# Kernel tuning notes

Hardware: AMD Instinct MI355X
Metric: run time of the kernel (lower is better)

Reference implementation:

```python
import jax, jax.numpy as jnp
import numpy as np

B, L, D = 32, 8192, 256
M = L // 2 + 1  # max possible valley count (strict local minima can't be adjacent)


def setup_inputs() -> dict:
    key = jax.random.key(0)
    k1, k2, k3 = jax.random.split(key, 3)
    xs_pad = jax.random.normal(k1, (B, L, D), dtype=jnp.float32)
    olens = jax.random.randint(k2, (B,), 1, L + 1, dtype=jnp.int32)
    # linear_sigmoid params: Linear(256, 1)
    W = jax.random.normal(k3, (D, 1), dtype=jnp.float32) * 0.05
    b = jnp.zeros((1,), dtype=jnp.float32)
    return {"xs_pad": xs_pad, "olens": olens, "W": W, "b": b}


def reference(xs_pad, olens, W, b):
    Bq, Lq, Dq = xs_pad.shape
    # scalar importance: sigmoid(Linear(x))  [B, L, 1]
    s = jax.nn.sigmoid(xs_pad @ W + b)
    alpha_h = s * xs_pad                       # [B, L, D]
    sq = s[..., 0]                             # [B, L]
    # shifted neighbors, zero-padded at the ends (matches F.pad of the detached scalars)
    s_before = jnp.pad(sq[:, :-1], ((0, 0), (1, 0)))
    s_after = jnp.pad(sq[:, 1:], ((0, 0), (0, 1)))
    mask = (sq < s_before) & (sq < s_after)    # strict local minima
    mask = mask.at[:, 0].set(True)             # first frame forced to be a valley start
    counts = mask.sum(axis=1).astype(jnp.int32)  # per-batch valley count (returned olens)

    # valley starts, sorted, padded with sentinel L  -> [B, M]
    pos = jnp.arange(Lq)
    starts = jnp.sort(jnp.where(mask, pos, Lq), axis=1)[:, :M]
    valid = (starts < Lq)
    # segment = [start, min(start+2, L)) i.e. frames start and start+1 (clipped)
    i0 = jnp.clip(starts, 0, Lq - 1)
    i1 = jnp.clip(starts + 1, 0, Lq - 1)
    w0 = valid.astype(xs_pad.dtype)[..., None]
    w1 = ((starts + 1 < Lq) & valid).astype(xs_pad.dtype)[..., None]

    def gather(a, idx):
        return jnp.take_along_axis(a, idx[:, :, None], axis=1)

    num = gather(alpha_h, i0) * w0 + gather(alpha_h, i1) * w1   # [B, M, D]
    den = gather(s, i0) * w0 + gather(s, i1) * w1               # [B, M, 1]
    out = num / jnp.maximum(den, 1e-6)
    return out, counts
```

## Files before the change

### kernel.cpp

```cpp
#include <hip/hip_runtime.h>
#include <math.h>

#define B_ 32
#define L_ 8192
#define D_ 256
#define M_ 4097

__global__ __launch_bounds__(256) void k_sigmoid_dot(
    const float* __restrict__ x, const float* __restrict__ W,
    const float* __restrict__ bias, float* __restrict__ s)
{
    int row  = (blockIdx.x << 2) + (threadIdx.x >> 6);
    int lane = threadIdx.x & 63;
    const float4 xv = ((const float4*)(x + (size_t)row * D_))[lane];
    const float4 wv = ((const float4*)W)[lane];
    float p = xv.x * wv.x + xv.y * wv.y + xv.z * wv.z + xv.w * wv.w;
#pragma unroll
    for (int off = 32; off > 0; off >>= 1)
        p += __shfl_xor(p, off, 64);
    if (lane == 0) {
        float z = p + bias[0];
        s[row] = 1.0f / (1.0f + expf(-z));
    }
}

__global__ __launch_bounds__(256) void k_scan(
    const float* __restrict__ s, int* __restrict__ starts,
    int* __restrict__ counts, float* __restrict__ out_counts)
{
    int b = blockIdx.x;
    const float* sb = s + (size_t)b * L_;
    int t    = threadIdx.x;
    int base = t * 32;

    unsigned bits = 0;
    int cnt = 0;
    float sprev = (base == 0) ? 0.0f : sb[base - 1];
    float sc    = sb[base];
#pragma unroll 1
    for (int i = 0; i < 32; i++) {
        int l = base + i;
        float snext = (l == L_ - 1) ? 0.0f : sb[l + 1];
        bool m = (l == 0) ? true : ((sc < sprev) && (sc < snext));
        if (m) { bits |= (1u << i); cnt++; }
        sprev = sc;
        sc    = snext;
    }

    __shared__ int sh[256];
    sh[t] = cnt;
    __syncthreads();
    for (int off = 1; off < 256; off <<= 1) {
        int v = (t >= off) ? sh[t - off] : 0;
        __syncthreads();
        sh[t] += v;
        __syncthreads();
    }
    int excl  = sh[t] - cnt;
    int total = sh[255];

    int k = excl;
    for (int i = 0; i < 32; i++) {
        if (bits & (1u << i)) { starts[b * M_ + k] = base + i; k++; }
    }
    if (t == 0) {
        counts[b]     = total;
        out_counts[b] = (float)total;
    }
}

__global__ __launch_bounds__(64) void k_write(
    const float* __restrict__ x, const float* __restrict__ s,
    const int* __restrict__ starts, const int* __restrict__ counts,
    float* __restrict__ out)
{
    int k    = blockIdx.x;
    int b    = blockIdx.y;
    int lane = threadIdx.x;
    float4* orow = (float4*)(out + ((size_t)b * M_ + k) * D_);
    if (k >= counts[b]) {
        orow[lane] = make_float4(0.f, 0.f, 0.f, 0.f);
        return;
    }
    int p = starts[b * M_ + k];
    const float* sb = s + (size_t)b * L_;
    float s0 = sb[p];
    bool has1 = (p + 1 < L_);
    float s1 = has1 ? sb[p + 1] : 0.0f;
    float inv = 1.0f / fmaxf(s0 + s1, 1e-6f);

    const float4* x0 = (const float4*)(x + ((size_t)b * L_ + p) * D_);
    float4 a = x0[lane];
    float4 r;
    r.x = s0 * a.x; r.y = s0 * a.y; r.z = s0 * a.z; r.w = s0 * a.w;
    if (has1) {
        float4 c = (x0 + (D_ / 4))[lane];
        r.x += s1 * c.x; r.y += s1 * c.y; r.z += s1 * c.z; r.w += s1 * c.w;
    }
    r.x *= inv; r.y *= inv; r.z *= inv; r.w *= inv;
    orow[lane] = r;
}

extern "C" void kernel_launch(void* const* d_in, const int* in_sizes, int n_in,
                              void* d_out, int out_size, void* d_ws, size_t ws_size,
                              hipStream_t stream) {
    const float* x    = (const float*)d_in[0];
    const float* W    = (const float*)d_in[2];
    const float* bias = (const float*)d_in[3];

    float* out        = (float*)d_out;
    float* out_counts = out + (size_t)B_ * M_ * D_;

    float* s      = (float*)d_ws;
    int*   starts = (int*)((char*)d_ws + (size_t)B_ * L_ * 4);
    int*   counts = (int*)((char*)starts + (size_t)B_ * M_ * 4);

    k_sigmoid_dot<<<(B_ * L_) / 4, 256, 0, stream>>>(x, W, bias, s);
    k_scan<<<B_, 256, 0, stream>>>(s, starts, counts, out_counts);
    k_write<<<dim3(M_, B_), 64, 0, stream>>>(x, s, starts, counts, out);
}
```

Measured before the change: 422.2 us.

## Batch rows per wave, vectorize scan loads, use nontemporal stores in write kernel

The sigmoid-dot kernel now has each wave handle four rows, issuing all loads up front so more memory traffic is in flight. The scan kernel loads its 32-element chunk with float4 reads into registers and fully unrolls the minima test. The write kernel uses 256-thread blocks that each cover eight output rows and writes them with nontemporal stores, which cuts block count and avoids polluting the cache with streamed output. The changes trade register pressure and larger blocks for fewer launches and better memory-level parallelism.

```diff
diff --git a/kernel.cpp b/kernel.cpp
--- a/kernel.cpp
+++ b/kernel.cpp
@@ -6,21 +6,31 @@
 #define D_ 256
 #define M_ 4097
 
+typedef float floatx4 __attribute__((ext_vector_type(4)));
+
 __global__ __launch_bounds__(256) void k_sigmoid_dot(
     const float* __restrict__ x, const float* __restrict__ W,
     const float* __restrict__ bias, float* __restrict__ s)
 {
-    int row  = (blockIdx.x << 2) + (threadIdx.x >> 6);
+    int wave = threadIdx.x >> 6;
     int lane = threadIdx.x & 63;
-    const float4 xv = ((const float4*)(x + (size_t)row * D_))[lane];
+    int row0 = blockIdx.x * 16 + wave * 4;
+
     const float4 wv = ((const float4*)W)[lane];
-    float p = xv.x * wv.x + xv.y * wv.y + xv.z * wv.z + xv.w * wv.w;
+    float4 xv[4];
 #pragma unroll
-    for (int off = 32; off > 0; off >>= 1)
-        p += __shfl_xor(p, off, 64);
-    if (lane == 0) {
-        float z = p + bias[0];
-        s[row] = 1.0f / (1.0f + expf(-z));
+    for (int i = 0; i < 4; i++)
+        xv[i] = ((const float4*)(x + (size_t)(row0 + i) * D_))[lane];
+    float zb = bias[0];
+
+#pragma unroll
+    for (int i = 0; i < 4; i++) {
+        float p = xv[i].x * wv.x + xv[i].y * wv.y + xv[i].z * wv.z + xv[i].w * wv.w;
+#pragma unroll
+        for (int off = 32; off > 0; off >>= 1)
+            p += __shfl_xor(p, off, 64);
+        if (lane == 0)
+            s[row0 + i] = 1.0f / (1.0f + expf(-(p + zb)));
     }
 }
 
@@ -33,18 +43,22 @@
     int t    = threadIdx.x;
     int base = t * 32;
 
+    float f[34];
+    f[0]  = (t == 0)   ? 0.0f : sb[base - 1];
+    f[33] = (t == 255) ? 0.0f : sb[base + 32];
+#pragma unroll
+    for (int i = 0; i < 8; i++) {
+        float4 q = ((const float4*)(sb + base))[i];
+        f[1 + 4 * i] = q.x; f[2 + 4 * i] = q.y;
+        f[3 + 4 * i] = q.z; f[4 + 4 * i] = q.w;
+    }
+
     unsigned bits = 0;
     int cnt = 0;
-    float sprev = (base == 0) ? 0.0f : sb[base - 1];
-    float sc    = sb[base];
-#pragma unroll 1
+#pragma unroll
     for (int i = 0; i < 32; i++) {
-        int l = base + i;
-        float snext = (l == L_ - 1) ? 0.0f : sb[l + 1];
-        bool m = (l == 0) ? true : ((sc < sprev) && (sc < snext));
+        bool m = ((f[i + 1] < f[i]) && (f[i + 1] < f[i + 2])) || (base + i == 0);
         if (m) { bits |= (1u << i); cnt++; }
-        sprev = sc;
-        sc    = snext;
     }
 
     __shared__ int sh[256];
@@ -69,36 +83,49 @@
     }
 }
 
-__global__ __launch_bounds__(64) void k_write(
+__device__ __forceinline__ void nt_store4(float* p, float4 v) {
+    floatx4 nv = { v.x, v.y, v.z, v.w };
+    __builtin_nontemporal_store(nv, (floatx4*)p);
+}
+
+__global__ __launch_bounds__(256) void k_write(
     const float* __restrict__ x, const float* __restrict__ s,
     const int* __restrict__ starts, const int* __restrict__ counts,
     float* __restrict__ out)
 {
-    int k    = blockIdx.x;
+    int wave = threadIdx.x >> 6;
+    int lane = threadIdx.x & 63;
     int b    = blockIdx.y;
-    int lane = threadIdx.x;
-    float4* orow = (float4*)(out + ((size_t)b * M_ + k) * D_);
-    if (k >= counts[b]) {
-        orow[lane] = make_float4(0.f, 0.f, 0.f, 0.f);
-        return;
+    int k0   = (blockIdx.x * 4 + wave) * 2;
+    int cnt  = counts[b];
+    const float* sb = s + (size_t)b * L_;
+
+#pragma unroll
+    for (int j = 0; j < 2; j++) {
+        int k = k0 + j;
+        if (k >= M_) continue;
+        float* orow = out + ((size_t)b * M_ + k) * D_ + lane * 4;
+        if (k >= cnt) {
+            nt_store4(orow, make_float4(0.f, 0.f, 0.f, 0.f));
+            continue;
+        }
+        int p = starts[b * M_ + k];
+        float s0 = sb[p];
+        bool has1 = (p + 1 < L_);
+        float s1 = has1 ? sb[p + 1] : 0.0f;
+        float inv = 1.0f / fmaxf(s0 + s1, 1e-6f);
+
+        const float4* x0 = (const float4*)(x + ((size_t)b * L_ + p) * D_);
+        float4 a = x0[lane];
+        float4 r;
+        r.x = s0 * a.x; r.y = s0 * a.y; r.z = s0 * a.z; r.w = s0 * a.w;
+        if (has1) {
+            float4 c = (x0 + (D_ / 4))[lane];
+            r.x += s1 * c.x; r.y += s1 * c.y; r.z += s1 * c.z; r.w += s1 * c.w;
+        }
+        r.x *= inv; r.y *= inv; r.z *= inv; r.w *= inv;
+        nt_store4(orow, r);
     }
-    int p = starts[b * M_ + k];
-    const float* sb = s + (size_t)b * L_;
-    float s0 = sb[p];
-    bool has1 = (p + 1 < L_);
-    float s1 = has1 ? sb[p + 1] : 0.0f;
-    float inv = 1.0f / fmaxf(s0 + s1, 1e-6f);
-
-    const float4* x0 = (const float4*)(x + ((size_t)b * L_ + p) * D_);
-    float4 a = x0[lane];
-    float4 r;
-    r.x = s0 * a.x; r.y = s0 * a.y; r.z = s0 * a.z; r.w = s0 * a.w;
-    if (has1) {
-        float4 c = (x0 + (D_ / 4))[lane];
-        r.x += s1 * c.x; r.y += s1 * c.y; r.z += s1 * c.z; r.w += s1 * c.w;
-    }
-    r.x *= inv; r.y *= inv; r.z *= inv; r.w *= inv;
-    orow[lane] = r;
 }
 
 extern "C" void kernel_launch(void* const* d_in, const int* in_sizes, int n_in,
@@ -115,7 +142,7 @@
     int*   starts = (int*)((char*)d_ws + (size_t)B_ * L_ * 4);
     int*   counts = (int*)((char*)starts + (size_t)B_ * M_ * 4);
 
-    k_sigmoid_dot<<<(B_ * L_) / 4, 256, 0, stream>>>(x, W, bias, s);
+    k_sigmoid_dot<<<(B_ * L_) / 16, 256, 0, stream>>>(x, W, bias, s);
     k_scan<<<B_, 256, 0, stream>>>(s, starts, counts, out_counts);
-    k_write<<<dim3(M_, B_), 64, 0, stream>>>(x, s, starts, counts, out);
+    k_write<<<dim3((M_ + 7) / 8, B_), 256, 0, stream>>>(x, s, starts, counts, out);
 }
```

Measured after the change: 423.9 us. No clear change (+0.4%).
